# Kernel optimization log

Measured on AMD Instinct MI355X. Metric: run time of the kernel, lower is better.

Reference implementation:

```python
import jax, jax.numpy as jnp
import numpy as np

N = 100000       # nodes
DEG = 16         # fixed out/in degree used to build CSR
E = N * DEG      # edges
D_IN = 128       # in_feats
D_OUT = 256      # out_feats
K = 32           # maxk k_value


def _xavier_uniform(key, shape, gain):
    fan_out, fan_in = shape
    bound = gain * np.sqrt(6.0 / (fan_in + fan_out))
    return jax.random.uniform(key, shape, jnp.float32, -bound, bound)


def setup_inputs() -> dict:
    key = jax.random.key(0)
    ks = jax.random.split(key, 6)
    feat = jax.random.normal(ks[0], (N, D_IN), jnp.float32)
    topk_values = jax.random.uniform(ks[1], (N, K), jnp.float32)
    topk_indices = jax.random.randint(ks[2], (N, K), 0, D_IN).astype(jnp.int32)
    # CSR graph: fixed degree -> indptr is arange*DEG; random destinations
    indptr = (jnp.arange(N + 1) * DEG).astype(jnp.int32)
    indices = jax.random.randint(ks[3], (E,), 0, N).astype(jnp.int32)
    # set_graph_data: csr weight[e] = 1 / clamp(in_degree(dst), 1)
    in_deg = jax.ops.segment_sum(jnp.ones(E, jnp.float32), indices, num_segments=N)
    in_deg = jnp.maximum(in_deg, 1.0)
    csr_values = 1.0 / in_deg[indices]
    gain = np.sqrt(2.0)  # calculate_gain('relu')
    w_neigh = _xavier_uniform(ks[4], (D_OUT, D_IN), gain)
    w_self = _xavier_uniform(ks[5], (D_OUT, D_IN), gain)
    b_self = jnp.zeros((D_OUT,), jnp.float32)
    return {"feat": feat, "topk_values": topk_values, "csr_values": csr_values,
            "w_neigh": w_neigh, "w_self": w_self, "b_self": b_self,
            "topk_indices": topk_indices, "indptr": indptr, "indices": indices}


def reference(feat, topk_values, csr_values, w_neigh, w_self, b_self,
              topk_indices, indptr, indices):
    # Densify the k-sparse MaxK features: x[n, topk_indices[n, j]] = topk_values[n, j]
    x = jnp.zeros((N, D_IN), feat.dtype).at[
        jnp.arange(N)[:, None], topk_indices].add(topk_values)
    # Edge-weight-normalized SpMM over CSR: out[row] += w[e] * x[col[e]]
    row_ids = jnp.repeat(jnp.arange(N), jnp.diff(indptr), total_repeat_length=E)
    msgs = x[indices] * csr_values[:, None]          # [E, D_IN]
    agg = jax.ops.segment_sum(msgs, row_ids, num_segments=N)  # [N, D_IN]
    # lin_before_mp is False (in_feats <= out_feats): project after aggregation
    h_neigh = agg @ w_neigh.T                        # [N, D_OUT]
    rst = feat @ w_self.T + b_self + h_neigh         # fc_self(h_self) + h_neigh
    return rst
```

## Files before the change

kernel.cpp:

```cpp
#include <hip/hip_runtime.h>
#include <hip/hip_bf16.h>
#include <stdint.h>

#define N_NODES 100000
#define DEG 16
#define D_IN 128
#define D_OUT 256
#define K_TOP 32
#define K_CAT 256

typedef __attribute__((ext_vector_type(8))) short short8;
typedef __attribute__((ext_vector_type(4))) float floatx4;

__device__ __forceinline__ unsigned pack_bf16_rne(float f) {
    union { float f; unsigned u; } c; c.f = f;
    unsigned u = c.u;
    return (u + 0x7fffu + ((u >> 16) & 1u)) >> 16;
}
__device__ __forceinline__ float bf16lo_to_f(unsigned lo16) {
    union { unsigned u; float f; } c; c.u = lo16 << 16; return c.f;
}

__global__ __launch_bounds__(256) void k_packw(const float* __restrict__ w_self,
                                               const float* __restrict__ w_neigh,
                                               unsigned short* __restrict__ bmat) {
    int o = blockIdx.x;
    int k = threadIdx.x;
    float v = (k < D_IN) ? w_self[o * D_IN + k] : w_neigh[o * D_IN + (k - D_IN)];
    bmat[o * K_CAT + k] = (unsigned short)pack_bf16_rne(v);
}

__global__ __launch_bounds__(256) void k_densify(const float* __restrict__ topk_v,
                                                 const int* __restrict__ topk_i,
                                                 const float* __restrict__ feat,
                                                 unsigned short* __restrict__ xbf,
                                                 unsigned short* __restrict__ abf) {
    int wave = threadIdx.x >> 6;
    int lane = threadIdx.x & 63;
    int row  = blockIdx.x * 4 + wave;
    if (row >= N_NODES) return;

    int   ix = 0; float v = 0.f;
    if (lane < K_TOP) {
        ix = topk_i[row * K_TOP + lane];
        v  = topk_v[row * K_TOP + lane];
    }
    const int c0 = 2 * lane, c1 = 2 * lane + 1;
    float a0 = 0.f, a1 = 0.f;
    #pragma unroll
    for (int j = 0; j < K_TOP; ++j) {
        int   idx = __shfl(ix, j);
        float val = __shfl(v, j);
        a0 += (idx == c0) ? val : 0.f;
        a1 += (idx == c1) ? val : 0.f;
    }
    unsigned xp = pack_bf16_rne(a0) | (pack_bf16_rne(a1) << 16);
    ((unsigned*)(xbf + (size_t)row * D_IN))[lane] = xp;

    const float2 f2 = *(const float2*)(feat + (size_t)row * D_IN + c0);
    unsigned fp = pack_bf16_rne(f2.x) | (pack_bf16_rne(f2.y) << 16);
    ((unsigned*)(abf + (size_t)row * K_CAT))[lane] = fp;
}

__global__ __launch_bounds__(256) void k_spmm(const float* __restrict__ csr_w,
                                              const int* __restrict__ col_idx,
                                              const unsigned short* __restrict__ xbf,
                                              unsigned short* __restrict__ abf) {
    int wave = threadIdx.x >> 6;
    int lane = threadIdx.x & 63;
    int row  = blockIdx.x * 4 + wave;
    if (row >= N_NODES) return;

    int c = 0; float w = 0.f;
    if (lane < DEG) {
        c = col_idx[row * DEG + lane];
        w = csr_w[row * DEG + lane];
    }
    unsigned vv[DEG];
    #pragma unroll
    for (int e = 0; e < DEG; ++e) {
        int col = __shfl(c, e);
        vv[e] = ((const unsigned*)(xbf + (size_t)col * D_IN))[lane];
    }
    float a0 = 0.f, a1 = 0.f;
    #pragma unroll
    for (int e = 0; e < DEG; ++e) {
        float we = __shfl(w, e);
        a0 += we * bf16lo_to_f(vv[e] & 0xffffu);
        a1 += we * bf16lo_to_f(vv[e] >> 16);
    }
    unsigned ap = pack_bf16_rne(a0) | (pack_bf16_rne(a1) << 16);
    ((unsigned*)(abf + (size_t)row * K_CAT + D_IN))[lane] = ap;
}

#define BM 128
#define BN 256
#define BK 32
#define LDP 40

__global__ __launch_bounds__(256, 2) void k_gemm(const unsigned short* __restrict__ abf,
                                                 const unsigned short* __restrict__ bmat,
                                                 const float* __restrict__ bias,
                                                 float* __restrict__ out) {
    __shared__ unsigned short As[BM * LDP];
    __shared__ unsigned short Bs[BN * LDP];
    int t = threadIdx.x;
    int lane = t & 63, wave = t >> 6;
    int wr = wave >> 1, wc = wave & 1;
    int row0 = blockIdx.x * BM;

    floatx4 acc[4][8];
    #pragma unroll
    for (int i = 0; i < 4; ++i)
        #pragma unroll
        for (int j = 0; j < 8; ++j)
            acc[i][j] = (floatx4){0.f, 0.f, 0.f, 0.f};

    int quad = lane >> 4;
    int l16  = lane & 15;

    for (int kt = 0; kt < K_CAT; kt += BK) {
        __syncthreads();
        #pragma unroll
        for (int p = 0; p < 2; ++p) {
            int chunk = t + p * 256;
            int r  = chunk >> 2;
            int ko = (chunk & 3) * 8;
            uint4 av = make_uint4(0u, 0u, 0u, 0u);
            int gr = row0 + r;
            if (gr < N_NODES)
                av = *(const uint4*)(abf + (size_t)gr * K_CAT + kt + ko);
            *(uint4*)&As[r * LDP + ko] = av;
        }
        #pragma unroll
        for (int p = 0; p < 4; ++p) {
            int chunk = t + p * 256;
            int r  = chunk >> 2;
            int ko = (chunk & 3) * 8;
            uint4 bv = *(const uint4*)(bmat + (size_t)r * K_CAT + kt + ko);
            *(uint4*)&Bs[r * LDP + ko] = bv;
        }
        __syncthreads();

        short8 afr[4], bfr[8];
        #pragma unroll
        for (int i = 0; i < 4; ++i) {
            int m = wr * 64 + i * 16 + l16;
            afr[i] = *(const short8*)&As[m * LDP + quad * 8];
        }
        #pragma unroll
        for (int j = 0; j < 8; ++j) {
            int n = wc * 128 + j * 16 + l16;
            bfr[j] = *(const short8*)&Bs[n * LDP + quad * 8];
        }
        #pragma unroll
        for (int i = 0; i < 4; ++i)
            #pragma unroll
            for (int j = 0; j < 8; ++j)
                acc[i][j] = __builtin_amdgcn_mfma_f32_16x16x32_bf16(afr[i], bfr[j], acc[i][j], 0, 0, 0);
    }

    #pragma unroll
    for (int j = 0; j < 8; ++j) {
        int cg = wc * 128 + j * 16 + l16;
        float bv = bias[cg];
        #pragma unroll
        for (int i = 0; i < 4; ++i) {
            int mbase = row0 + wr * 64 + i * 16 + quad * 4;
            #pragma unroll
            for (int r = 0; r < 4; ++r) {
                int gr = mbase + r;
                if (gr < N_NODES) out[(size_t)gr * D_OUT + cg] = acc[i][j][r] + bv;
            }
        }
    }
}

extern "C" void kernel_launch(void* const* d_in, const int* in_sizes, int n_in,
                              void* d_out, int out_size, void* d_ws, size_t ws_size,
                              hipStream_t stream) {
    const float* feat    = (const float*)d_in[0];
    const float* topk_v  = (const float*)d_in[1];
    const float* csr_w   = (const float*)d_in[2];
    const float* w_neigh = (const float*)d_in[3];
    const float* w_self  = (const float*)d_in[4];
    const float* b_self  = (const float*)d_in[5];
    const int*   topk_i  = (const int*)d_in[6];
    const int*   indices = (const int*)d_in[8];
    float* out = (float*)d_out;

    unsigned short* xbf  = (unsigned short*)d_ws;
    unsigned short* abf  = xbf + (size_t)N_NODES * D_IN;
    unsigned short* bmat = abf + (size_t)N_NODES * K_CAT;

    k_packw<<<dim3(256), dim3(256), 0, stream>>>(w_self, w_neigh, bmat);
    k_densify<<<dim3(N_NODES / 4), dim3(256), 0, stream>>>(topk_v, topk_i, feat, xbf, abf);
    k_spmm<<<dim3(N_NODES / 4), dim3(256), 0, stream>>>(csr_w, indices, xbf, abf);
    k_gemm<<<dim3((N_NODES + BM - 1) / BM), dim3(256), 0, stream>>>(abf, bmat, b_self, out);
}
```

Before: 325.2 us.

## Densify via LDS atomics over row tiles and widen SpMM gathers to 8 bytes

Densify now stages a 64-row tile in shared memory. It scatters the top-k values into that tile with LDS atomicAdd instead of doing a 32-step shuffle-compare loop per row, then writes packed bf16 rows with wider stores. The feat conversion also moves to float4 loads. SpMM now processes two rows per wave, with each half-wave gathering 8 bytes per lane per neighbour, which halves the number of gather instructions. The risks are LDS atomic contention and heavier shared-memory use, which may lower occupancy.

```diff
diff --git a/kernel.cpp b/kernel.cpp
--- a/kernel.cpp
+++ b/kernel.cpp
@@ -30,67 +30,97 @@
     bmat[o * K_CAT + k] = (unsigned short)pack_bf16_rne(v);
 }
 
+#define DROWS 64
 __global__ __launch_bounds__(256) void k_densify(const float* __restrict__ topk_v,
                                                  const int* __restrict__ topk_i,
                                                  const float* __restrict__ feat,
                                                  unsigned short* __restrict__ xbf,
                                                  unsigned short* __restrict__ abf) {
-    int wave = threadIdx.x >> 6;
-    int lane = threadIdx.x & 63;
-    int row  = blockIdx.x * 4 + wave;
-    if (row >= N_NODES) return;
-
-    int   ix = 0; float v = 0.f;
-    if (lane < K_TOP) {
-        ix = topk_i[row * K_TOP + lane];
-        v  = topk_v[row * K_TOP + lane];
-    }
-    const int c0 = 2 * lane, c1 = 2 * lane + 1;
-    float a0 = 0.f, a1 = 0.f;
-    #pragma unroll
-    for (int j = 0; j < K_TOP; ++j) {
-        int   idx = __shfl(ix, j);
-        float val = __shfl(v, j);
-        a0 += (idx == c0) ? val : 0.f;
-        a1 += (idx == c1) ? val : 0.f;
-    }
-    unsigned xp = pack_bf16_rne(a0) | (pack_bf16_rne(a1) << 16);
-    ((unsigned*)(xbf + (size_t)row * D_IN))[lane] = xp;
-
-    const float2 f2 = *(const float2*)(feat + (size_t)row * D_IN + c0);
-    unsigned fp = pack_bf16_rne(f2.x) | (pack_bf16_rne(f2.y) << 16);
-    ((unsigned*)(abf + (size_t)row * K_CAT))[lane] = fp;
+    __shared__ float sx[DROWS * D_IN];
+    const int t = threadIdx.x;
+    const int row0 = blockIdx.x * DROWS;
+
+    #pragma unroll
+    for (int p = 0; p < 8; ++p)
+        *(floatx4*)&sx[(t + p * 256) * 4] = (floatx4){0.f, 0.f, 0.f, 0.f};
+    __syncthreads();
+
+    const size_t tbase = (size_t)row0 * K_TOP;
+    #pragma unroll
+    for (int p = 0; p < 8; ++p) {
+        int q = t + p * 256;
+        int r = q >> 5;
+        if (row0 + r < N_NODES) {
+            int   ci = topk_i[tbase + q];
+            float cv = topk_v[tbase + q];
+            atomicAdd(&sx[r * D_IN + ci], cv);
+        }
+    }
+    __syncthreads();
+
+    #pragma unroll
+    for (int p = 0; p < 16; ++p) {
+        int d = t + p * 256;
+        int r = d >> 6;
+        int c2 = (d & 63) * 2;
+        if (row0 + r < N_NODES) {
+            float2 v = *(const float2*)&sx[r * D_IN + c2];
+            ((unsigned*)(xbf + (size_t)(row0 + r) * D_IN))[d & 63] =
+                pack_bf16_rne(v.x) | (pack_bf16_rne(v.y) << 16);
+        }
+    }
+
+    #pragma unroll
+    for (int p = 0; p < 8; ++p) {
+        int q = t + p * 256;
+        int r = q >> 5;
+        int c4 = (q & 31) * 4;
+        if (row0 + r < N_NODES) {
+            float4 f = *(const float4*)(feat + (size_t)(row0 + r) * D_IN + c4);
+            uint2 pk;
+            pk.x = pack_bf16_rne(f.x) | (pack_bf16_rne(f.y) << 16);
+            pk.y = pack_bf16_rne(f.z) | (pack_bf16_rne(f.w) << 16);
+            ((uint2*)(abf + (size_t)(row0 + r) * K_CAT))[q & 31] = pk;
+        }
+    }
 }
 
 __global__ __launch_bounds__(256) void k_spmm(const float* __restrict__ csr_w,
                                               const int* __restrict__ col_idx,
                                               const unsigned short* __restrict__ xbf,
                                               unsigned short* __restrict__ abf) {
-    int wave = threadIdx.x >> 6;
-    int lane = threadIdx.x & 63;
-    int row  = blockIdx.x * 4 + wave;
+    const int wave = threadIdx.x >> 6;
+    const int lane = threadIdx.x & 63;
+    const int pair = blockIdx.x * 4 + wave;
+    const int row  = 2 * pair + (lane >> 5);
+    const int hl   = lane & 31;
     if (row >= N_NODES) return;
 
     int c = 0; float w = 0.f;
-    if (lane < DEG) {
-        c = col_idx[row * DEG + lane];
-        w = csr_w[row * DEG + lane];
-    }
-    unsigned vv[DEG];
+    if (hl < DEG) {
+        c = col_idx[row * DEG + hl];
+        w = csr_w[row * DEG + hl];
+    }
+    const int bsel = lane & 32;
+    uint2 vv[DEG];
     #pragma unroll
     for (int e = 0; e < DEG; ++e) {
-        int col = __shfl(c, e);
-        vv[e] = ((const unsigned*)(xbf + (size_t)col * D_IN))[lane];
-    }
-    float a0 = 0.f, a1 = 0.f;
+        int col = __shfl(c, bsel | e);
+        vv[e] = *(const uint2*)(xbf + (size_t)col * D_IN + hl * 4);
+    }
+    float a0 = 0.f, a1 = 0.f, a2 = 0.f, a3 = 0.f;
     #pragma unroll
     for (int e = 0; e < DEG; ++e) {
-        float we = __shfl(w, e);
-        a0 += we * bf16lo_to_f(vv[e] & 0xffffu);
-        a1 += we * bf16lo_to_f(vv[e] >> 16);
-    }
-    unsigned ap = pack_bf16_rne(a0) | (pack_bf16_rne(a1) << 16);
-    ((unsigned*)(abf + (size_t)row * K_CAT + D_IN))[lane] = ap;
+        float we = __shfl(w, bsel | e);
+        a0 += we * bf16lo_to_f(vv[e].x & 0xffffu);
+        a1 += we * bf16lo_to_f(vv[e].x >> 16);
+        a2 += we * bf16lo_to_f(vv[e].y & 0xffffu);
+        a3 += we * bf16lo_to_f(vv[e].y >> 16);
+    }
+    uint2 pk;
+    pk.x = pack_bf16_rne(a0) | (pack_bf16_rne(a1) << 16);
+    pk.y = pack_bf16_rne(a2) | (pack_bf16_rne(a3) << 16);
+    ((uint2*)(abf + (size_t)row * K_CAT + D_IN))[hl] = pk;
 }
 
 #define BM 128
@@ -194,7 +224,7 @@
     unsigned short* bmat = abf + (size_t)N_NODES * K_CAT;
 
     k_packw<<<dim3(256), dim3(256), 0, stream>>>(w_self, w_neigh, bmat);
-    k_densify<<<dim3(N_NODES / 4), dim3(256), 0, stream>>>(topk_v, topk_i, feat, xbf, abf);
-    k_spmm<<<dim3(N_NODES / 4), dim3(256), 0, stream>>>(csr_w, indices, xbf, abf);
+    k_densify<<<dim3((N_NODES + DROWS - 1) / DROWS), dim3(256), 0, stream>>>(topk_v, topk_i, feat, xbf, abf);
+    k_spmm<<<dim3((N_NODES + 7) / 8), dim3(256), 0, stream>>>(csr_w, indices, xbf, abf);
     k_gemm<<<dim3((N_NODES + BM - 1) / BM), dim3(256), 0, stream>>>(abf, bmat, b_self, out);
 }
```

Result: faster. 308.2 us (-5.2%).
